# Optimization experiments

Hardware: AMD Instinct MI355X
Metric: run time of the kernel (lower is better)

Reference implementation:

```python
import jax, jax.numpy as jnp
import numpy as np

EMBED_DIM = 1024
NUM_HEADS = 16
HEAD_DIM = EMBED_DIM // NUM_HEADS


def setup_inputs() -> dict:
    key = jax.random.key(0)
    ks = jax.random.split(key, 9)
    B, S, D = 2, 2048, EMBED_DIM
    scale = 1.0 / np.sqrt(D)
    x = jax.random.normal(ks[0], (B, S, D), dtype=jnp.float32)
    Wq = jax.random.normal(ks[1], (D, D), dtype=jnp.float32) * scale
    Wk = jax.random.normal(ks[2], (D, D), dtype=jnp.float32) * scale
    Wv = jax.random.normal(ks[3], (D, D), dtype=jnp.float32) * scale
    Wo = jax.random.normal(ks[4], (D, D), dtype=jnp.float32) * scale
    bq = jnp.zeros((D,), jnp.float32)
    bk = jnp.zeros((D,), jnp.float32)
    bv = jnp.zeros((D,), jnp.float32)
    bo = jnp.zeros((D,), jnp.float32)
    return {"x": x, "Wq": Wq, "bq": bq, "Wk": Wk, "bk": bk,
            "Wv": Wv, "bv": bv, "Wo": Wo, "bo": bo}


def reference(x, Wq, bq, Wk, bk, Wv, bv, Wo, bo):
    B, S, D = x.shape
    H, Dh = NUM_HEADS, HEAD_DIM
    # QKV projections -> [B, H, S, Dh]
    q = (x @ Wq + bq).reshape(B, S, H, Dh).transpose(0, 2, 1, 3)
    k = (x @ Wk + bk).reshape(B, S, H, Dh).transpose(0, 2, 1, 3)
    v = (x @ Wv + bv).reshape(B, S, H, Dh).transpose(0, 2, 1, 3)
    # scores [B, H, S, S], scaled by sqrt(head_dim)
    scores = jnp.einsum('bhqd,bhkd->bhqk', q, k) / jnp.sqrt(jnp.float32(Dh))
    attn = jax.nn.softmax(scores, axis=-1)
    out = jnp.einsum('bhqk,bhkd->bhqd', attn, v)  # [B, H, S, Dh]
    out = out.transpose(0, 2, 1, 3).reshape(B, S, D)
    return out @ Wo + bo
```

## Files before the change

### kernel.cpp

```cpp
#include <hip/hip_runtime.h>
#include <hip/hip_bf16.h>

typedef short bf16x8 __attribute__((ext_vector_type(8)));
typedef float f32x4 __attribute__((ext_vector_type(4)));
typedef unsigned uint2v __attribute__((ext_vector_type(2)));

#define MFMA16(a, b, c) __builtin_amdgcn_mfma_f32_16x16x32_bf16((a), (b), (c), 0, 0, 0)

#if __has_builtin(__builtin_amdgcn_exp2f)
#define EXP2(x) __builtin_amdgcn_exp2f(x)
#else
#define EXP2(x) exp2f(x)
#endif

static constexpr int B_ = 2, S_ = 2048, D_ = 1024, H_ = 16, DH = 64;
static constexpr int M_ = B_ * S_;
static constexpr int K_ = D_;
static constexpr float kQS = 0.18033688011112042f;

static __device__ __forceinline__ ushort f2bf(float f) {
    __hip_bfloat16 h = __float2bfloat16(f);
    return *reinterpret_cast<ushort*>(&h);
}
static __device__ __forceinline__ float bf2f(ushort u) {
    __hip_bfloat16 h;
    *reinterpret_cast<ushort*>(&h) = u;
    return __bfloat162float(h);
}

static __device__ __forceinline__ void gload16(const ushort* g, ushort* l) {
    __builtin_amdgcn_global_load_lds((const __attribute__((address_space(1))) void*)g,
                                     (__attribute__((address_space(3))) void*)l, 16, 0, 0);
}

static __device__ __forceinline__ unsigned pkbf(float lo, float hi) {
    return __builtin_amdgcn_perm(__builtin_bit_cast(unsigned, hi),
                                 __builtin_bit_cast(unsigned, lo), 0x07060302u);
}

__global__ __launch_bounds__(256) void prep5(const float* __restrict__ x,
                                             const float* __restrict__ W0,
                                             const float* __restrict__ W1,
                                             const float* __restrict__ W2,
                                             const float* __restrict__ W3,
                                             ushort* __restrict__ xb,
                                             ushort* __restrict__ T0,
                                             ushort* __restrict__ T1,
                                             ushort* __restrict__ T2,
                                             ushort* __restrict__ T3) {
    int z = blockIdx.z;
    int tx = threadIdx.x, ty = threadIdx.y;
    int t = ty * 32 + tx;
    if (z == 4) {
        int blk = blockIdx.y * 32 + blockIdx.x;
#pragma unroll
        for (int k = 0; k < 4; k++) {
            int i = blk * 1024 + k * 256 + t;
            float4 v = reinterpret_cast<const float4*>(x)[i];
            ushort4 o;
            o.x = f2bf(v.x); o.y = f2bf(v.y); o.z = f2bf(v.z); o.w = f2bf(v.w);
            reinterpret_cast<ushort4*>(xb)[i] = o;
        }
        return;
    }
    __shared__ float tile[32][33];
    const float* W = (z == 0) ? W0 : (z == 1) ? W1 : (z == 2) ? W2 : W3;
    ushort* T = (z == 0) ? T0 : (z == 1) ? T1 : (z == 2) ? T2 : T3;
    float sc = (z == 0) ? kQS : 1.0f;
    int bx = blockIdx.x, by = blockIdx.y;
#pragma unroll
    for (int i = 0; i < 4; i++)
        tile[ty + i * 8][tx] = W[(by * 32 + ty + i * 8) * D_ + bx * 32 + tx];
    __syncthreads();
#pragma unroll
    for (int i = 0; i < 4; i++)
        T[(bx * 32 + ty + i * 8) * K_ + by * 32 + tx] = f2bf(tile[tx][ty + i * 8] * sc);
}

template <int MODE, int TN>
__global__ __launch_bounds__(256, 3) void gemm128(const ushort* __restrict__ A,
                                                  const ushort* __restrict__ Wt,
                                                  const float* __restrict__ bias_q,
                                                  const float* __restrict__ bias_k,
                                                  const float* __restrict__ bias_v,
                                                  ushort* __restrict__ Qb,
                                                  ushort* __restrict__ Kb,
                                                  ushort* __restrict__ Vtb,
                                                  float* __restrict__ outf) {
    constexpr int NJ = TN / 32;
    __shared__ __align__(16) ushort As[128 * 32];
    __shared__ __align__(16) ushort Bs[TN * 32];

    int m0 = blockIdx.x * 128;
    int n0 = blockIdx.y * TN;
    int t = threadIdx.x;
    int lane = t & 63, w = t >> 6;
    int ln = lane & 15, lq = lane >> 4;
    int wm = (w >> 1) * 64, wn = (w & 1) * (TN / 2);

    int c0 = t, c1 = t + 256;
    const ushort* Ag0 = A + (size_t)(m0 + (c0 >> 2)) * K_ + (c0 & 3) * 8;
    const ushort* Ag1 = A + (size_t)(m0 + (c1 >> 2)) * K_ + (c1 & 3) * 8;
    const ushort* Bg0 = Wt + (size_t)(n0 + (c0 >> 2)) * K_ + (c0 & 3) * 8;
    const ushort* Bg1 = Wt + (size_t)(n0 + (c1 >> 2)) * K_ + (c1 & 3) * 8;
    ushort* Al0 = As + c0 * 8;
    ushort* Al1 = As + c1 * 8;
    ushort* Bl0 = Bs + c0 * 8;
    ushort* Bl1 = Bs + c1 * 8;

    const bool swp = (MODE == 1) || (n0 < 2048);

    f32x4 acc[4][NJ];
#pragma unroll
    for (int i = 0; i < 4; i++)
#pragma unroll
        for (int j = 0; j < NJ; j++) acc[i][j] = f32x4{0.f, 0.f, 0.f, 0.f};

    if (swp) {
        for (int k0 = 0; k0 < K_; k0 += 32) {
            gload16(Ag0 + k0, Al0);
            gload16(Ag1 + k0, Al1);
            gload16(Bg0 + k0, Bl0);
            if (TN == 128) gload16(Bg1 + k0, Bl1);
            __syncthreads();
            bf16x8 af[4], bfr[NJ];
#pragma unroll
            for (int i = 0; i < 4; i++)
                af[i] = *reinterpret_cast<const bf16x8*>(As + (wm + i * 16 + ln) * 32 + lq * 8);
#pragma unroll
            for (int j = 0; j < NJ; j++)
                bfr[j] = *reinterpret_cast<const bf16x8*>(Bs + (wn + j * 16 + ln) * 32 + lq * 8);
#pragma unroll
            for (int i = 0; i < 4; i++)
#pragma unroll
                for (int j = 0; j < NJ; j++)
                    acc[i][j] = MFMA16(bfr[j], af[i], acc[i][j]);
            __syncthreads();
        }
    } else {
        for (int k0 = 0; k0 < K_; k0 += 32) {
            gload16(Ag0 + k0, Al0);
            gload16(Ag1 + k0, Al1);
            gload16(Bg0 + k0, Bl0);
            if (TN == 128) gload16(Bg1 + k0, Bl1);
            __syncthreads();
            bf16x8 af[4], bfr[NJ];
#pragma unroll
            for (int i = 0; i < 4; i++)
                af[i] = *reinterpret_cast<const bf16x8*>(As + (wm + i * 16 + ln) * 32 + lq * 8);
#pragma unroll
            for (int j = 0; j < NJ; j++)
                bfr[j] = *reinterpret_cast<const bf16x8*>(Bs + (wn + j * 16 + ln) * 32 + lq * 8);
#pragma unroll
            for (int i = 0; i < 4; i++)
#pragma unroll
                for (int j = 0; j < NJ; j++)
                    acc[i][j] = MFMA16(af[i], bfr[j], acc[i][j]);
            __syncthreads();
        }
    }

    if (MODE == 1) {
#pragma unroll
        for (int j = 0; j < NJ; j++) {
            int nb = n0 + wn + j * 16 + lq * 4;
            float4 bv4 = *reinterpret_cast<const float4*>(bias_q + nb);
#pragma unroll
            for (int i = 0; i < 4; i++) {
                int m = m0 + wm + i * 16 + ln;
                float4 o;
                o.x = acc[i][j][0] + bv4.x;
                o.y = acc[i][j][1] + bv4.y;
                o.z = acc[i][j][2] + bv4.z;
                o.w = acc[i][j][3] + bv4.w;
                *reinterpret_cast<float4*>(outf + (size_t)m * D_ + nb) = o;
            }
        }
    } else if (n0 < 2048) {
        int which = n0 >> 10;
        const float* bp = which ? bias_k : bias_q;
        ushort* dst = which ? Kb : Qb;
        float bsc = which ? 1.0f : kQS;
#pragma unroll
        for (int j = 0; j < NJ; j++) {
            int nb = ((n0 + wn + j * 16) & 1023) + lq * 4;
            int h = nb >> 6, dhb = nb & 63;
            float4 bv4 = *reinterpret_cast<const float4*>(bp + nb);
            bv4.x *= bsc; bv4.y *= bsc; bv4.z *= bsc; bv4.w *= bsc;
#pragma unroll
            for (int i = 0; i < 4; i++) {
                int m = m0 + wm + i * 16 + ln;
                int b = m >> 11, s = m & 2047;
                ushort4 o4;
                o4.x = f2bf(acc[i][j][0] + bv4.x);
                o4.y = f2bf(acc[i][j][1] + bv4.y);
                o4.z = f2bf(acc[i][j][2] + bv4.z);
                o4.w = f2bf(acc[i][j][3] + bv4.w);
                *reinterpret_cast<ushort4*>(dst + (((size_t)(b * H_ + h) * S_) + s) * DH + dhb) = o4;
            }
        }
    } else {
#pragma unroll
        for (int j = 0; j < NJ; j++) {
            int n = n0 + wn + j * 16 + ln;
            int nn = n & 1023, h = nn >> 6, dh = nn & 63;
            float bv = bias_v[nn];
#pragma unroll
            for (int i = 0; i < 4; i++) {
                int m = m0 + wm + i * 16 + lq * 4;
                int b = m >> 11, s0 = m & 2047;
                ushort4 o4;
                o4.x = f2bf(acc[i][j][0] + bv);
                o4.y = f2bf(acc[i][j][1] + bv);
                o4.z = f2bf(acc[i][j][2] + bv);
                o4.w = f2bf(acc[i][j][3] + bv);
                *reinterpret_cast<ushort4*>(Vtb + (((size_t)(b * H_ + h) * DH) + dh) * S_ + s0) = o4;
            }
        }
    }
}

__global__ __launch_bounds__(256, 4) void attn128s(const ushort* __restrict__ Q,
                                                   const ushort* __restrict__ K,
                                                   const ushort* __restrict__ Vt,
                                                   ushort* __restrict__ O1,
                                                   ushort* __restrict__ O2,
                                                   float* __restrict__ L) {
    __shared__ __align__(16) ushort Kl[512 * 8];
    __shared__ __align__(16) ushort Vl[512 * 8];
    __shared__ __align__(16) ushort Pl[4][2][16 * 72];

    int bid = blockIdx.x;
    int half = bid >> 9;
    int rem = bid & 511;
    int qb = rem & 15;
    int bh = rem >> 4;
    int t = threadIdx.x;
    int lane = t & 63, w = t >> 6;
    int ln = lane & 15, lq = lane >> 4;
    int q0 = qb * 128 + w * 32;

    const ushort* Qp = Q + (size_t)bh * S_ * DH;
    const ushort* Kp = K + (size_t)bh * S_ * DH + (size_t)half * 1024 * DH;
    const ushort* Vp = Vt + (size_t)bh * DH * S_ + (size_t)half * 1024;

    bf16x8 qf[2][2];
#pragma unroll
    for (int tl = 0; tl < 2; tl++) {
        const ushort* qp = Qp + (q0 + tl * 16 + ln) * DH + lq * 8;
        qf[tl][0] = *reinterpret_cast<const bf16x8*>(qp);
        qf[tl][1] = *reinterpret_cast<const bf16x8*>(qp + 32);
    }

    bf16x8 ones;
#pragma unroll
    for (int j = 0; j < 8; j++) ones[j] = (short)0x3F80;

    int c0 = t, c1 = t + 256;
    const ushort* Kg0 = Kp + (size_t)(c0 & 63) * DH + (c0 >> 6) * 8;
    const ushort* Kg1 = Kp + (size_t)(c1 & 63) * DH + (c1 >> 6) * 8;
    const ushort* Vg0 = Vp + (size_t)(c0 & 63) * S_ + (c0 >> 6) * 8;
    const ushort* Vg1 = Vp + (size_t)(c1 & 63) * S_ + (c1 >> 6) * 8;
    ushort* Kl0 = Kl + c0 * 8;
    ushort* Kl1 = Kl + c1 * 8;
    ushort* Vl0 = Vl + c0 * 8;
    ushort* Vl1 = Vl + c1 * 8;

    f32x4 o_acc[2][4];
    f32x4 l_acc[2];
#pragma unroll
    for (int tl = 0; tl < 2; tl++) {
        l_acc[tl] = f32x4{0.f, 0.f, 0.f, 0.f};
#pragma unroll
        for (int nt = 0; nt < 4; nt++) o_acc[tl][nt] = f32x4{0.f, 0.f, 0.f, 0.f};
    }

    for (int kt = 0; kt < 16; kt++) {
        int kb = kt * 64;
        gload16(Kg0 + (size_t)kb * DH, Kl0);
        gload16(Kg1 + (size_t)kb * DH, Kl1);
        gload16(Vg0 + kb, Vl0);
        gload16(Vg1 + kb, Vl1);
        __syncthreads();

        f32x4 sc[2][4];
#pragma unroll
        for (int nt = 0; nt < 4; nt++) {
            bf16x8 kf0 = *reinterpret_cast<const bf16x8*>(Kl + (lq * 64 + nt * 16 + ln) * 8);
            bf16x8 kf1 = *reinterpret_cast<const bf16x8*>(Kl + ((4 + lq) * 64 + nt * 16 + ln) * 8);
#pragma unroll
            for (int tl = 0; tl < 2; tl++) {
                f32x4 c = {0.f, 0.f, 0.f, 0.f};
                c = MFMA16(kf0, qf[tl][0], c);
                c = MFMA16(kf1, qf[tl][1], c);
                sc[tl][nt] = c;
            }
        }
#pragma unroll
        for (int tl = 0; tl < 2; tl++)
#pragma unroll
            for (int nt = 0; nt < 4; nt++) {
                float p0 = EXP2(sc[tl][nt][0]);
                float p1 = EXP2(sc[tl][nt][1]);
                float p2 = EXP2(sc[tl][nt][2]);
                float p3 = EXP2(sc[tl][nt][3]);
                uint2v pk;
                pk.x = pkbf(p0, p1);
                pk.y = pkbf(p2, p3);
                *reinterpret_cast<uint2v*>(&Pl[w][tl][ln * 72 + nt * 16 + lq * 4]) = pk;
            }
        bf16x8 pf[2][2];
#pragma unroll
        for (int tl = 0; tl < 2; tl++) {
            pf[tl][0] = *reinterpret_cast<const bf16x8*>(&Pl[w][tl][ln * 72 + lq * 8]);
            pf[tl][1] = *reinterpret_cast<const bf16x8*>(&Pl[w][tl][ln * 72 + 32 + lq * 8]);
            l_acc[tl] = MFMA16(pf[tl][0], ones, l_acc[tl]);
            l_acc[tl] = MFMA16(pf[tl][1], ones, l_acc[tl]);
        }
#pragma unroll
        for (int nt = 0; nt < 4; nt++) {
            bf16x8 vf0 = *reinterpret_cast<const bf16x8*>(Vl + (lq * 64 + nt * 16 + ln) * 8);
            bf16x8 vf1 = *reinterpret_cast<const bf16x8*>(Vl + ((4 + lq) * 64 + nt * 16 + ln) * 8);
#pragma unroll
            for (int tl = 0; tl < 2; tl++) {
                o_acc[tl][nt] = MFMA16(pf[tl][0], vf0, o_acc[tl][nt]);
                o_acc[tl][nt] = MFMA16(pf[tl][1], vf1, o_acc[tl][nt]);
            }
        }
        __syncthreads();
    }

    ushort* Op = half ? O2 : O1;
    float* Lp = L + ((size_t)half * 32 + bh) * S_;
    int b = bh >> 4, h = bh & 15;
#pragma unroll
    for (int tl = 0; tl < 2; tl++) {
        float linv[4];
#pragma unroll
        for (int r = 0; r < 4; r++) {
            linv[r] = 1.0f / l_acc[tl][r];
            if (ln == 0) Lp[q0 + tl * 16 + lq * 4 + r] = l_acc[tl][r];
        }
#pragma unroll
        for (int nt = 0; nt < 4; nt++)
#pragma unroll
            for (int r = 0; r < 4; r++) {
                int s = q0 + tl * 16 + lq * 4 + r;
                Op[((b * S_ + s) * H_ + h) * DH + nt * 16 + ln] =
                    f2bf(o_acc[tl][nt][r] * linv[r]);
            }
    }
}

__global__ __launch_bounds__(256) void attn_comb(const ushort* __restrict__ O1,
                                                 const ushort* __restrict__ O2,
                                                 const float* __restrict__ L,
                                                 ushort* __restrict__ AO) {
    int i = blockIdx.x * 256 + threadIdx.x;
    int row = i >> 7;
    int col = (i & 127) * 8;
    int h = col >> 6;
    int b = row >> 11, s = row & 2047;
    int bh = b * 16 + h;
    float l1 = L[(size_t)bh * S_ + s];
    float l2 = L[((size_t)32 + bh) * S_ + s];
    float inv = 1.0f / (l1 + l2);
    float w1 = l1 * inv, w2 = l2 * inv;
    size_t off = (size_t)row * D_ + col;
    ushort4 a0 = reinterpret_cast<const ushort4*>(O1 + off)[0];
    ushort4 a1 = reinterpret_cast<const ushort4*>(O1 + off)[1];
    ushort4 b0 = reinterpret_cast<const ushort4*>(O2 + off)[0];
    ushort4 b1 = reinterpret_cast<const ushort4*>(O2 + off)[1];
    ushort4 o0, o1v;
    o0.x = f2bf(w1 * bf2f(a0.x) + w2 * bf2f(b0.x));
    o0.y = f2bf(w1 * bf2f(a0.y) + w2 * bf2f(b0.y));
    o0.z = f2bf(w1 * bf2f(a0.z) + w2 * bf2f(b0.z));
    o0.w = f2bf(w1 * bf2f(a0.w) + w2 * bf2f(b0.w));
    o1v.x = f2bf(w1 * bf2f(a1.x) + w2 * bf2f(b1.x));
    o1v.y = f2bf(w1 * bf2f(a1.y) + w2 * bf2f(b1.y));
    o1v.z = f2bf(w1 * bf2f(a1.z) + w2 * bf2f(b1.z));
    o1v.w = f2bf(w1 * bf2f(a1.w) + w2 * bf2f(b1.w));
    reinterpret_cast<ushort4*>(AO + off)[0] = o0;
    reinterpret_cast<ushort4*>(AO + off)[1] = o1v;
}

extern "C" void kernel_launch(void* const* d_in, const int* in_sizes, int n_in,
                              void* d_out, int out_size, void* d_ws, size_t ws_size,
                              hipStream_t stream) {
    const float* x  = (const float*)d_in[0];
    const float* Wq = (const float*)d_in[1];
    const float* bq = (const float*)d_in[2];
    const float* Wk = (const float*)d_in[3];
    const float* bk = (const float*)d_in[4];
    const float* Wv = (const float*)d_in[5];
    const float* bv = (const float*)d_in[6];
    const float* Wo = (const float*)d_in[7];
    const float* bo = (const float*)d_in[8];
    float* out = (float*)d_out;

    char* ws = (char*)d_ws;
    const size_t MB = 1024 * 1024;
    ushort* wtq = (ushort*)(ws + 0 * MB);
    ushort* wtk = (ushort*)(ws + 2 * MB);
    ushort* wtv = (ushort*)(ws + 4 * MB);
    ushort* wto = (ushort*)(ws + 6 * MB);
    ushort* xb  = (ushort*)(ws + 8 * MB);
    ushort* Qb  = (ushort*)(ws + 16 * MB);
    ushort* Kb  = (ushort*)(ws + 24 * MB);
    ushort* Vtb = (ushort*)(ws + 32 * MB);
    ushort* AO  = (ushort*)(ws + 40 * MB);
    ushort* O1  = (ushort*)(ws + 8 * MB);
    ushort* O2  = (ushort*)(ws + 48 * MB);
    float*  Lw  = (float*)(ws + 56 * MB);

    prep5<<<dim3(32, 32, 5), dim3(32, 8), 0, stream>>>(
        x, Wq, Wk, Wv, Wo, xb, wtq, wtk, wtv, wto);

    gemm128<0, 128><<<dim3(M_ / 128, 3072 / 128), 256, 0, stream>>>(
        xb, wtq, bq, bk, bv, Qb, Kb, Vtb, nullptr);

    attn128s<<<1024, 256, 0, stream>>>(Qb, Kb, Vtb, O1, O2, Lw);
    attn_comb<<<(M_ * D_ / 8) / 256, 256, 0, stream>>>(O1, O2, Lw, AO);

    gemm128<1, 64><<<dim3(M_ / 128, D_ / 64), 256, 0, stream>>>(
        AO, wto, bo, nullptr, nullptr, nullptr, nullptr, nullptr, out);
}
```

Baseline: 194.7 us.

## Rewrite attention with 32x32 MFMA, permlane P transpose, and double-buffered K/V

The attention kernel moves from 16x16x32 MFMA tiles to 32x32x16 MFMA tiles, so each wave computes a 32-query by 32-key score block. The P matrix is repacked in registers with permlane32_swap instead of a round trip through shared memory. K/V tiles are double-buffered in LDS, prefetching the next tile while the current one is computed, which drops one barrier per iteration. The intent is to remove LDS traffic and sync stalls at the cost of larger LDS usage and higher register pressure.

```diff
diff --git a/kernel.cpp b/kernel.cpp
--- a/kernel.cpp
+++ b/kernel.cpp
@@ -3,9 +3,12 @@
 
 typedef short bf16x8 __attribute__((ext_vector_type(8)));
 typedef float f32x4 __attribute__((ext_vector_type(4)));
+typedef float f32x16 __attribute__((ext_vector_type(16)));
 typedef unsigned uint2v __attribute__((ext_vector_type(2)));
+typedef unsigned uint4v __attribute__((ext_vector_type(4)));
 
 #define MFMA16(a, b, c) __builtin_amdgcn_mfma_f32_16x16x32_bf16((a), (b), (c), 0, 0, 0)
+#define MFMA32(a, b, c) __builtin_amdgcn_mfma_f32_32x32x16_bf16((a), (b), (c), 0, 0, 0)
 
 #if __has_builtin(__builtin_amdgcn_exp2f)
 #define EXP2(x) __builtin_amdgcn_exp2f(x)
@@ -220,15 +223,14 @@
     }
 }
 
-__global__ __launch_bounds__(256, 4) void attn128s(const ushort* __restrict__ Q,
-                                                   const ushort* __restrict__ K,
-                                                   const ushort* __restrict__ Vt,
-                                                   ushort* __restrict__ O1,
-                                                   ushort* __restrict__ O2,
-                                                   float* __restrict__ L) {
-    __shared__ __align__(16) ushort Kl[512 * 8];
-    __shared__ __align__(16) ushort Vl[512 * 8];
-    __shared__ __align__(16) ushort Pl[4][2][16 * 72];
+__global__ __launch_bounds__(256, 4) void attn32(const ushort* __restrict__ Q,
+                                                 const ushort* __restrict__ K,
+                                                 const ushort* __restrict__ Vt,
+                                                 ushort* __restrict__ O1,
+                                                 ushort* __restrict__ O2,
+                                                 float* __restrict__ L) {
+    __shared__ __align__(16) ushort Kl[2][4096];
+    __shared__ __align__(16) ushort Vl[2][4096];
 
     int bid = blockIdx.x;
     int half = bid >> 9;
@@ -237,20 +239,17 @@
     int bh = rem >> 4;
     int t = threadIdx.x;
     int lane = t & 63, w = t >> 6;
-    int ln = lane & 15, lq = lane >> 4;
+    int ln = lane & 31, hi = lane >> 5;
     int q0 = qb * 128 + w * 32;
 
     const ushort* Qp = Q + (size_t)bh * S_ * DH;
     const ushort* Kp = K + (size_t)bh * S_ * DH + (size_t)half * 1024 * DH;
     const ushort* Vp = Vt + (size_t)bh * DH * S_ + (size_t)half * 1024;
 
-    bf16x8 qf[2][2];
-#pragma unroll
-    for (int tl = 0; tl < 2; tl++) {
-        const ushort* qp = Qp + (q0 + tl * 16 + ln) * DH + lq * 8;
-        qf[tl][0] = *reinterpret_cast<const bf16x8*>(qp);
-        qf[tl][1] = *reinterpret_cast<const bf16x8*>(qp + 32);
-    }
+    bf16x8 qf[4];
+#pragma unroll
+    for (int ks = 0; ks < 4; ks++)
+        qf[ks] = *reinterpret_cast<const bf16x8*>(Qp + (size_t)(q0 + ln) * DH + ks * 16 + hi * 8);
 
     bf16x8 ones;
 #pragma unroll
@@ -261,94 +260,79 @@
     const ushort* Kg1 = Kp + (size_t)(c1 & 63) * DH + (c1 >> 6) * 8;
     const ushort* Vg0 = Vp + (size_t)(c0 & 63) * S_ + (c0 >> 6) * 8;
     const ushort* Vg1 = Vp + (size_t)(c1 & 63) * S_ + (c1 >> 6) * 8;
-    ushort* Kl0 = Kl + c0 * 8;
-    ushort* Kl1 = Kl + c1 * 8;
-    ushort* Vl0 = Vl + c0 * 8;
-    ushort* Vl1 = Vl + c1 * 8;
-
-    f32x4 o_acc[2][4];
-    f32x4 l_acc[2];
-#pragma unroll
-    for (int tl = 0; tl < 2; tl++) {
-        l_acc[tl] = f32x4{0.f, 0.f, 0.f, 0.f};
-#pragma unroll
-        for (int nt = 0; nt < 4; nt++) o_acc[tl][nt] = f32x4{0.f, 0.f, 0.f, 0.f};
-    }
+
+    f32x16 o_acc[2];
+    f32x16 l_acc;
+#pragma unroll
+    for (int r = 0; r < 16; r++) { o_acc[0][r] = 0.f; o_acc[1][r] = 0.f; l_acc[r] = 0.f; }
+
+    gload16(Kg0, &Kl[0][c0 * 8]);
+    gload16(Kg1, &Kl[0][c1 * 8]);
+    gload16(Vg0, &Vl[0][c0 * 8]);
+    gload16(Vg1, &Vl[0][c1 * 8]);
 
     for (int kt = 0; kt < 16; kt++) {
-        int kb = kt * 64;
-        gload16(Kg0 + (size_t)kb * DH, Kl0);
-        gload16(Kg1 + (size_t)kb * DH, Kl1);
-        gload16(Vg0 + kb, Vl0);
-        gload16(Vg1 + kb, Vl1);
+        int cur = kt & 1;
         __syncthreads();
-
-        f32x4 sc[2][4];
-#pragma unroll
-        for (int nt = 0; nt < 4; nt++) {
-            bf16x8 kf0 = *reinterpret_cast<const bf16x8*>(Kl + (lq * 64 + nt * 16 + ln) * 8);
-            bf16x8 kf1 = *reinterpret_cast<const bf16x8*>(Kl + ((4 + lq) * 64 + nt * 16 + ln) * 8);
-#pragma unroll
-            for (int tl = 0; tl < 2; tl++) {
-                f32x4 c = {0.f, 0.f, 0.f, 0.f};
-                c = MFMA16(kf0, qf[tl][0], c);
-                c = MFMA16(kf1, qf[tl][1], c);
-                sc[tl][nt] = c;
+        if (kt < 15) {
+            int kb = (kt + 1) * 64;
+            gload16(Kg0 + (size_t)kb * DH, &Kl[cur ^ 1][c0 * 8]);
+            gload16(Kg1 + (size_t)kb * DH, &Kl[cur ^ 1][c1 * 8]);
+            gload16(Vg0 + kb, &Vl[cur ^ 1][c0 * 8]);
+            gload16(Vg1 + kb, &Vl[cur ^ 1][c1 * 8]);
+        }
+        const ushort* Kc = Kl[cur];
+        const ushort* Vc = Vl[cur];
+#pragma unroll
+        for (int kb2 = 0; kb2 < 2; kb2++) {
+            f32x16 sc;
+#pragma unroll
+            for (int r = 0; r < 16; r++) sc[r] = 0.f;
+#pragma unroll
+            for (int ks = 0; ks < 4; ks++) {
+                bf16x8 kf = *reinterpret_cast<const bf16x8*>(
+                    Kc + (ks * 2 + hi) * 512 + (kb2 * 32 + ln) * 8);
+                sc = MFMA32(kf, qf[ks], sc);
             }
-        }
-#pragma unroll
-        for (int tl = 0; tl < 2; tl++)
-#pragma unroll
-            for (int nt = 0; nt < 4; nt++) {
-                float p0 = EXP2(sc[tl][nt][0]);
-                float p1 = EXP2(sc[tl][nt][1]);
-                float p2 = EXP2(sc[tl][nt][2]);
-                float p3 = EXP2(sc[tl][nt][3]);
-                uint2v pk;
-                pk.x = pkbf(p0, p1);
-                pk.y = pkbf(p2, p3);
-                *reinterpret_cast<uint2v*>(&Pl[w][tl][ln * 72 + nt * 16 + lq * 4]) = pk;
+            unsigned pk[8];
+#pragma unroll
+            for (int j = 0; j < 8; j++)
+                pk[j] = pkbf(EXP2(sc[2 * j]), EXP2(sc[2 * j + 1]));
+            uint2v s0 = __builtin_amdgcn_permlane32_swap(pk[0], pk[2], false, false);
+            uint2v s1 = __builtin_amdgcn_permlane32_swap(pk[1], pk[3], false, false);
+            uint2v s2 = __builtin_amdgcn_permlane32_swap(pk[4], pk[6], false, false);
+            uint2v s3 = __builtin_amdgcn_permlane32_swap(pk[5], pk[7], false, false);
+            bf16x8 f0 = __builtin_bit_cast(bf16x8, (uint4v){s0.x, s1.x, s0.y, s1.y});
+            bf16x8 f1 = __builtin_bit_cast(bf16x8, (uint4v){s2.x, s3.x, s2.y, s3.y});
+            l_acc = MFMA32(f0, ones, l_acc);
+            l_acc = MFMA32(f1, ones, l_acc);
+#pragma unroll
+            for (int h2 = 0; h2 < 2; h2++) {
+                bf16x8 v0 = *reinterpret_cast<const bf16x8*>(
+                    Vc + (kb2 * 4 + hi) * 512 + (h2 * 32 + ln) * 8);
+                bf16x8 v1 = *reinterpret_cast<const bf16x8*>(
+                    Vc + (kb2 * 4 + 2 + hi) * 512 + (h2 * 32 + ln) * 8);
+                o_acc[h2] = MFMA32(f0, v0, o_acc[h2]);
+                o_acc[h2] = MFMA32(f1, v1, o_acc[h2]);
             }
-        bf16x8 pf[2][2];
-#pragma unroll
-        for (int tl = 0; tl < 2; tl++) {
-            pf[tl][0] = *reinterpret_cast<const bf16x8*>(&Pl[w][tl][ln * 72 + lq * 8]);
-            pf[tl][1] = *reinterpret_cast<const bf16x8*>(&Pl[w][tl][ln * 72 + 32 + lq * 8]);
-            l_acc[tl] = MFMA16(pf[tl][0], ones, l_acc[tl]);
-            l_acc[tl] = MFMA16(pf[tl][1], ones, l_acc[tl]);
-        }
-#pragma unroll
-        for (int nt = 0; nt < 4; nt++) {
-            bf16x8 vf0 = *reinterpret_cast<const bf16x8*>(Vl + (lq * 64 + nt * 16 + ln) * 8);
-            bf16x8 vf1 = *reinterpret_cast<const bf16x8*>(Vl + ((4 + lq) * 64 + nt * 16 + ln) * 8);
-#pragma unroll
-            for (int tl = 0; tl < 2; tl++) {
-                o_acc[tl][nt] = MFMA16(pf[tl][0], vf0, o_acc[tl][nt]);
-                o_acc[tl][nt] = MFMA16(pf[tl][1], vf1, o_acc[tl][nt]);
-            }
-        }
-        __syncthreads();
+        }
     }
 
     ushort* Op = half ? O2 : O1;
     float* Lp = L + ((size_t)half * 32 + bh) * S_;
     int b = bh >> 4, h = bh & 15;
-#pragma unroll
-    for (int tl = 0; tl < 2; tl++) {
-        float linv[4];
-#pragma unroll
-        for (int r = 0; r < 4; r++) {
-            linv[r] = 1.0f / l_acc[tl][r];
-            if (ln == 0) Lp[q0 + tl * 16 + lq * 4 + r] = l_acc[tl][r];
-        }
-#pragma unroll
-        for (int nt = 0; nt < 4; nt++)
-#pragma unroll
-            for (int r = 0; r < 4; r++) {
-                int s = q0 + tl * 16 + lq * 4 + r;
-                Op[((b * S_ + s) * H_ + h) * DH + nt * 16 + ln] =
-                    f2bf(o_acc[tl][nt][r] * linv[r]);
-            }
+    if (ln == 0) {
+#pragma unroll
+        for (int r = 0; r < 16; r++)
+            Lp[q0 + (r & 3) + 8 * (r >> 2) + 4 * hi] = l_acc[r];
+    }
+#pragma unroll
+    for (int r = 0; r < 16; r++) {
+        int s = q0 + (r & 3) + 8 * (r >> 2) + 4 * hi;
+        float linv = 1.0f / l_acc[r];
+        size_t base = (((size_t)(b * S_ + s)) * H_ + h) * DH;
+        Op[base + ln] = f2bf(o_acc[0][r] * linv);
+        Op[base + 32 + ln] = f2bf(o_acc[1][r] * linv);
     }
 }
 
@@ -419,7 +403,7 @@
     gemm128<0, 128><<<dim3(M_ / 128, 3072 / 128), 256, 0, stream>>>(
         xb, wtq, bq, bk, bv, Qb, Kb, Vtb, nullptr);
 
-    attn128s<<<1024, 256, 0, stream>>>(Qb, Kb, Vtb, O1, O2, Lw);
+    attn32<<<1024, 256, 0, stream>>>(Qb, Kb, Vtb, O1, O2, Lw);
     attn_comb<<<(M_ * D_ / 8) / 256, 256, 0, stream>>>(O1, O2, Lw, AO);
 
     gemm128<1, 64><<<dim3(M_ / 128, D_ / 64), 256, 0, stream>>>(
```

Result: no change. 197.6 us (+1.5%).
